# Performance work log

Measured on AMD Instinct MI355X. Metric: run time of the kernel, lower is better.

The kernel has to match this reference:

```python
import jax, jax.numpy as jnp
import numpy as np

DIM = 1024
HEADS = 16
HEAD_DIM = DIM // HEADS


def setup_inputs() -> dict:
    key = jax.random.key(0)
    ks = jax.random.split(key, 9)
    x = jax.random.normal(ks[0], (2, 2048, DIM), dtype=jnp.float32)
    s = 1.0 / np.sqrt(DIM)
    Wq = jax.random.normal(ks[1], (DIM, DIM), dtype=jnp.float32) * s
    bq = jax.random.normal(ks[2], (DIM,), dtype=jnp.float32) * s
    Wk = jax.random.normal(ks[3], (DIM, DIM), dtype=jnp.float32) * s
    bk = jax.random.normal(ks[4], (DIM,), dtype=jnp.float32) * s
    Wv = jax.random.normal(ks[5], (DIM, DIM), dtype=jnp.float32) * s
    bv = jax.random.normal(ks[6], (DIM,), dtype=jnp.float32) * s
    Wo = jax.random.normal(ks[7], (DIM, DIM), dtype=jnp.float32) * s
    bo = jax.random.normal(ks[8], (DIM,), dtype=jnp.float32) * s
    return {"x": x, "Wq": Wq, "bq": bq, "Wk": Wk, "bk": bk,
            "Wv": Wv, "bv": bv, "Wo": Wo, "bo": bo}


def reference(x, Wq, bq, Wk, bk, Wv, bv, Wo, bo):
    B, S, _ = x.shape
    # projections (torch Linear: x @ W.T + b; here W stored as [in, out])
    q = x @ Wq + bq
    k = x @ Wk + bk  # context = x (self-attention)
    v = x @ Wv + bv
    # [B, H, S, Dh]
    q = q.reshape(B, S, HEADS, HEAD_DIM).transpose(0, 2, 1, 3)
    k = k.reshape(B, S, HEADS, HEAD_DIM).transpose(0, 2, 1, 3)
    v = v.reshape(B, S, HEADS, HEAD_DIM).transpose(0, 2, 1, 3)
    scores = jnp.einsum('bhqd,bhkd->bhqk', q, k) / np.sqrt(HEAD_DIM).astype(np.float32)
    weights = jax.nn.softmax(scores, axis=-1)
    emb = jnp.einsum('bhqk,bhkd->bhqd', weights, v)
    emb = emb.transpose(0, 2, 1, 3).reshape(B, S, DIM)
    return emb @ Wo + bo
```

## Files before the change

kernel.cpp:

```cpp
#include <hip/hip_runtime.h>
#include <hip/hip_bf16.h>
#include <stdint.h>

typedef __attribute__((ext_vector_type(8))) short short8;
typedef __attribute__((ext_vector_type(4))) float f32x4;
typedef __attribute__((ext_vector_type(4))) unsigned int uint4v;

#define DIMW 1024
#define HEADS 16
#define HEAD_DIM 64
#define SEQ 2048
#define BATCH 2
#define MTOK 4096
#define QKVN 3072
#define QKN 2048
#define QSCALE 0.1803368801111204f

typedef const __attribute__((address_space(1))) unsigned int* gas_u32p;
typedef __attribute__((address_space(3))) unsigned int* las_u32p;

static __device__ __forceinline__ void gl_lds16(const void* g, void* l) {
    __builtin_amdgcn_global_load_lds((gas_u32p)g, (las_u32p)l, 16, 0, 0);
}

static __device__ __forceinline__ unsigned short f2bf(float f) {
    unsigned int u = __float_as_uint(f);
    u += 0x7fffu + ((u >> 16) & 1u);
    return (unsigned short)(u >> 16);
}

__global__ void cast_x_kernel(const float* __restrict__ x, unsigned short* __restrict__ out) {
    int i = (blockIdx.x * 256 + threadIdx.x) * 8;
    float4 a = *(const float4*)(x + i);
    float4 b = *(const float4*)(x + i + 4);
    unsigned short t[8] = { f2bf(a.x), f2bf(a.y), f2bf(a.z), f2bf(a.w),
                            f2bf(b.x), f2bf(b.y), f2bf(b.z), f2bf(b.w) };
    *(uint4v*)(out + i) = *(const uint4v*)t;
}

__global__ void prep_w_kernel(const float* __restrict__ Wq, const float* __restrict__ Wk,
                              const float* __restrict__ Wv, const float* __restrict__ Wo,
                              unsigned short* __restrict__ Wqkv_t, unsigned short* __restrict__ Wo_t) {
    __shared__ float tile[64][68];
    int z = blockIdx.z;
    const float* W = (z == 0) ? Wq : (z == 1) ? Wk : (z == 2) ? Wv : Wo;
    unsigned short* out = (z < 3) ? (Wqkv_t + (size_t)z * DIMW * DIMW) : Wo_t;
    int n0 = blockIdx.x * 64, k0 = blockIdx.y * 64;
    int tid = threadIdx.x;
    for (int it = 0; it < 4; ++it) {
        int c = it * 256 + tid;
        int r = c >> 4, cg = c & 15;
        float4 v = *(const float4*)(W + (size_t)(k0 + r) * DIMW + n0 + cg * 4);
        tile[r][cg * 4 + 0] = v.x; tile[r][cg * 4 + 1] = v.y;
        tile[r][cg * 4 + 2] = v.z; tile[r][cg * 4 + 3] = v.w;
    }
    __syncthreads();
    for (int it = 0; it < 2; ++it) {
        int c = it * 256 + tid;
        int n = c >> 3, kg = c & 7;
        unsigned short tmp[8];
        #pragma unroll
        for (int j = 0; j < 8; ++j) tmp[j] = f2bf(tile[kg * 8 + j][n]);
        *(uint4v*)(out + (size_t)(n0 + n) * DIMW + k0 + kg * 8) = *(const uint4v*)tmp;
    }
}

template<int MI, bool QKV3, typename TO>
__global__ __launch_bounds__(256, 3) void gemm_bt_kernel(
    const unsigned short* __restrict__ A, const unsigned short* __restrict__ Bt,
    const float* __restrict__ b0, const float* __restrict__ b1, const float* __restrict__ b2,
    TO* __restrict__ C, unsigned short* __restrict__ Vt, int M, int N, int K, int ldc)
{
    __shared__ __align__(16) unsigned short As[MI * 32 * 32];
    __shared__ __align__(16) unsigned short Bs[128 * 32];
    int tid = threadIdx.x;
    int wave = tid >> 6, lane = tid & 63;
    int lrow = lane & 15, quad = lane >> 4;
    int bm = blockIdx.y * (MI * 32), bn = blockIdx.x * 128;
    int wm = (wave >> 1) * (MI * 16), wn = (wave & 1) * 64;
    int sw = (lrow >> 1) & 3;
    f32x4 acc[MI][4];
    #pragma unroll
    for (int i = 0; i < MI; ++i)
        #pragma unroll
        for (int j = 0; j < 4; ++j) acc[i][j] = (f32x4){0.f, 0.f, 0.f, 0.f};
    const unsigned short* Ap = A + (size_t)bm * K;
    const unsigned short* Bp = Bt + (size_t)bn * K;
    for (int k0 = 0; k0 < K; k0 += 32) {
        __syncthreads();
        #pragma unroll
        for (int it = 0; it < MI / 2; ++it) {
            int c = it * 256 + tid;
            int ch = (c & 3) ^ ((c >> 3) & 3);
            gl_lds16(Ap + (size_t)(c >> 2) * K + k0 + ch * 8, &As[c * 8]);
        }
        #pragma unroll
        for (int it = 0; it < 2; ++it) {
            int c = it * 256 + tid;
            int ch = (c & 3) ^ ((c >> 3) & 3);
            gl_lds16(Bp + (size_t)(c >> 2) * K + k0 + ch * 8, &Bs[c * 8]);
        }
        __syncthreads();
        short8 af[MI], bfr[4];
        #pragma unroll
        for (int mi = 0; mi < MI; ++mi)
            af[mi] = *(const short8*)&As[(wm + mi * 16 + lrow) * 32 + (quad ^ sw) * 8];
        #pragma unroll
        for (int ni = 0; ni < 4; ++ni)
            bfr[ni] = *(const short8*)&Bs[(wn + ni * 16 + lrow) * 32 + (quad ^ sw) * 8];
        #pragma unroll
        for (int mi = 0; mi < MI; ++mi)
            #pragma unroll
            for (int ni = 0; ni < 4; ++ni)
                acc[mi][ni] = __builtin_amdgcn_mfma_f32_16x16x32_bf16(af[mi], bfr[ni], acc[mi][ni], 0, 0, 0);
    }
    #pragma unroll
    for (int ni = 0; ni < 4; ++ni) {
        int n = bn + wn + ni * 16 + lrow;
        float bias, scale;
        int sel = 0;
        if (QKV3) {
            sel = n >> 10;
            const float* bp = (sel == 0) ? b0 : (sel == 1) ? b1 : b2;
            bias = bp[n & 1023];
            scale = (sel == 0) ? QSCALE : 1.0f;
        } else { bias = b0[n]; scale = 1.0f; }
        #pragma unroll
        for (int mi = 0; mi < MI; ++mi) {
            int m0 = bm + wm + mi * 16 + quad * 4;
            if (QKV3 && sel == 2) {
                int vcol = n - 2048;
                int bb = m0 >> 11, s0 = m0 & 2047;
                unsigned short t[4];
                #pragma unroll
                for (int i = 0; i < 4; ++i) t[i] = f2bf(acc[mi][ni][i] + bias);
                *(uint2*)(Vt + ((size_t)(bb * 1024 + vcol)) * SEQ + s0) = *(const uint2*)t;
            } else {
                #pragma unroll
                for (int i = 0; i < 4; ++i) {
                    float val = (acc[mi][ni][i] + bias) * scale;
                    if constexpr (sizeof(TO) == 2) C[(size_t)(m0 + i) * ldc + n] = (TO)f2bf(val);
                    else                           C[(size_t)(m0 + i) * ldc + n] = val;
                }
            }
        }
    }
}

__global__ __launch_bounds__(256, 3) void attn_kernel(
    const unsigned short* __restrict__ Qk, const unsigned short* __restrict__ Vt,
    unsigned short* __restrict__ Op, float* __restrict__ L)
{
    __shared__ __align__(16) unsigned short Ks[128 * 64];
    __shared__ __align__(16) unsigned short Vs[64 * 128];
    int tid = threadIdx.x;
    int wave = tid >> 6, lane = tid & 63;
    int lrow = lane & 15, quad = lane >> 4;
    int h = blockIdx.x, qblk = blockIdx.y;
    int b = blockIdx.z >> 1, split = blockIdx.z & 1;
    int q0 = qblk * 128 + wave * 32;
    const unsigned short* Qbase = Qk + (size_t)(b * SEQ) * QKN + h * 64;
    const unsigned short* Kbase = Qk + (size_t)(b * SEQ) * QKN + 1024 + h * 64;
    const unsigned short* Vtb = Vt + (size_t)(b * 1024 + h * 64) * SEQ;

    short8 qf[2][2];
    #pragma unroll
    for (int mi = 0; mi < 2; ++mi)
        #pragma unroll
        for (int kc = 0; kc < 2; ++kc)
            qf[mi][kc] = *(const short8*)(Qbase + (size_t)(q0 + mi * 16 + lrow) * QKN + kc * 32 + quad * 8);

    f32x4 o[2][4];
    float lrun[2] = {0.f, 0.f};
    #pragma unroll
    for (int mi = 0; mi < 2; ++mi)
        #pragma unroll
        for (int ont = 0; ont < 4; ++ont) o[mi][ont] = (f32x4){0.f, 0.f, 0.f, 0.f};

    int kchunk = ((lane & 7) ^ (lane >> 3)) * 8;
    int swk = lrow & 7;

    auto stageK = [&](int kv) {
        #pragma unroll
        for (int it = 0; it < 4; ++it) {
            int r0 = wave * 32 + it * 8;
            gl_lds16(Kbase + (size_t)(kv + r0 + (lane >> 3)) * QKN + kchunk,
                     &Ks[r0 * 64 + lane * 8]);
        }
    };

    int vs_s = lane & 15;
    int vh0 = ((vs_s & 12) << 1) | (vs_s & 3);
    uint2 vreg[8];
    auto loadV = [&](int kv) {
        #pragma unroll
        for (int r = 0; r < 4; ++r) {
            int d = wave * 16 + r * 4 + (lane >> 4);
            const unsigned short* p = Vtb + (size_t)d * SEQ + kv;
            vreg[r * 2]     = *(const uint2*)(p + vh0 * 4);
            vreg[r * 2 + 1] = *(const uint2*)(p + (vh0 + 4) * 4);
        }
    };
    auto writeVs = [&]() {
        #pragma unroll
        for (int r = 0; r < 4; ++r) {
            int d = wave * 16 + r * 4 + (lane >> 4);
            int pos = vs_s ^ (d & 15);
            uint4v w;
            w.x = vreg[r * 2].x;     w.y = vreg[r * 2].y;
            w.z = vreg[r * 2 + 1].x; w.w = vreg[r * 2 + 1].y;
            *(uint4v*)&Vs[d * 128 + pos * 8] = w;
        }
    };

    int kv_lo = split * 1024;
    int kv_end = kv_lo + 1024;

    stageK(kv_lo);
    loadV(kv_lo);
    asm volatile("s_waitcnt vmcnt(0)" ::: "memory");
    __builtin_amdgcn_sched_barrier(0);
    writeVs();

    for (int kv0 = kv_lo; kv0 < kv_end; kv0 += 128) {
        bool has_next = (kv0 + 128) < kv_end;

        __builtin_amdgcn_s_barrier();

        uint4v pav[2][4];
        #pragma unroll
        for (int half = 0; half < 2; ++half) {
            f32x4 s[2][4];
            #pragma unroll
            for (int mi = 0; mi < 2; ++mi)
                #pragma unroll
                for (int nt2 = 0; nt2 < 4; ++nt2) s[mi][nt2] = (f32x4){0.f, 0.f, 0.f, 0.f};
            __builtin_amdgcn_s_setprio(1);
            #pragma unroll
            for (int nt2 = 0; nt2 < 4; ++nt2) {
                int r = (half * 4 + nt2) * 16 + lrow;
                short8 kf0 = *(const short8*)&Ks[r * 64 + (quad ^ swk) * 8];
                short8 kf1 = *(const short8*)&Ks[r * 64 + ((4 + quad) ^ swk) * 8];
                #pragma unroll
                for (int mi = 0; mi < 2; ++mi) {
                    s[mi][nt2] = __builtin_amdgcn_mfma_f32_16x16x32_bf16(kf0, qf[mi][0], s[mi][nt2], 0, 0, 0);
                    s[mi][nt2] = __builtin_amdgcn_mfma_f32_16x16x32_bf16(kf1, qf[mi][1], s[mi][nt2], 0, 0, 0);
                }
            }
            __builtin_amdgcn_s_setprio(0);
            #pragma unroll
            for (int mi = 0; mi < 2; ++mi)
                #pragma unroll
                for (int nt2 = 0; nt2 < 4; ++nt2) {
                    int kt = half * 4 + nt2;
                    f32x4 p;
                    #pragma unroll
                    for (int c2 = 0; c2 < 4; ++c2) {
                        p[c2] = __builtin_amdgcn_exp2f(s[mi][nt2][c2]);
                        lrun[mi] += p[c2];
                    }
                    __hip_bfloat162 a01 = __float22bfloat162_rn(float2{p[0], p[1]});
                    __hip_bfloat162 a23 = __float22bfloat162_rn(float2{p[2], p[3]});
                    if (kt & 1) {
                        pav[mi][kt >> 1].z = *reinterpret_cast<unsigned int*>(&a01);
                        pav[mi][kt >> 1].w = *reinterpret_cast<unsigned int*>(&a23);
                    } else {
                        pav[mi][kt >> 1].x = *reinterpret_cast<unsigned int*>(&a01);
                        pav[mi][kt >> 1].y = *reinterpret_cast<unsigned int*>(&a23);
                    }
                }
        }

        __builtin_amdgcn_s_barrier();

        if (has_next) { stageK(kv0 + 128); loadV(kv0 + 128); }

        #pragma unroll
        for (int kc = 0; kc < 4; ++kc) {
            short8 af0 = *(short8*)&pav[0][kc];
            short8 af1 = *(short8*)&pav[1][kc];
            int pos = ((kc * 4 + quad) ^ lrow) * 8;
            __builtin_amdgcn_s_setprio(1);
            #pragma unroll
            for (int ont = 0; ont < 4; ++ont) {
                int rv = ont * 16 + lrow;
                short8 vf = *(const short8*)&Vs[rv * 128 + pos];
                o[0][ont] = __builtin_amdgcn_mfma_f32_16x16x32_bf16(af0, vf, o[0][ont], 0, 0, 0);
                o[1][ont] = __builtin_amdgcn_mfma_f32_16x16x32_bf16(af1, vf, o[1][ont], 0, 0, 0);
            }
            __builtin_amdgcn_s_setprio(0);
        }

        __builtin_amdgcn_s_barrier();

        if (has_next) {
            asm volatile("s_waitcnt vmcnt(0)" ::: "memory");
            __builtin_amdgcn_sched_barrier(0);
            writeVs();
        }
    }

    #pragma unroll
    for (int mi = 0; mi < 2; ++mi) {
        float l = lrun[mi];
        l += __shfl_xor(l, 16);
        l += __shfl_xor(l, 32);
        #pragma unroll
        for (int ont = 0; ont < 4; ++ont)
            #pragma unroll
            for (int c2 = 0; c2 < 4; ++c2) {
                size_t row = (size_t)((split * 2 + b) * SEQ + q0 + mi * 16 + quad * 4 + c2);
                Op[row * DIMW + h * 64 + ont * 16 + lrow] = f2bf(o[mi][ont][c2]);
            }
        if (quad == 0)
            L[(((size_t)(split * 2 + b) * 16 + h) * SEQ) + q0 + mi * 16 + lrow] = l;
    }
}

__global__ void combine_kernel(const unsigned short* __restrict__ Op,
                               const float* __restrict__ L,
                               unsigned short* __restrict__ Emb)
{
    int e = (blockIdx.x * 256 + threadIdx.x) * 4;
    int row = e >> 10, c = e & 1023, h = c >> 6;
    int b = row >> 11, q = row & 2047;
    float l1 = L[((size_t)(0 + b) * 16 + h) * SEQ + q];
    float l2 = L[((size_t)(2 + b) * 16 + h) * SEQ + q];
    float inv = 1.0f / (l1 + l2);
    uint2 o1 = *(const uint2*)(Op + e);
    uint2 o2 = *(const uint2*)(Op + 4194304 + e);
    unsigned short t[4];
    unsigned int parts1[4] = { o1.x << 16, o1.x & 0xffff0000u, o1.y << 16, o1.y & 0xffff0000u };
    unsigned int parts2[4] = { o2.x << 16, o2.x & 0xffff0000u, o2.y << 16, o2.y & 0xffff0000u };
    #pragma unroll
    for (int j = 0; j < 4; ++j) {
        float f1 = __uint_as_float(parts1[j]);
        float f2 = __uint_as_float(parts2[j]);
        t[j] = f2bf((f1 + f2) * inv);
    }
    *(uint2*)(Emb + e) = *(const uint2*)t;
}

extern "C" void kernel_launch(void* const* d_in, const int* in_sizes, int n_in,
                              void* d_out, int out_size, void* d_ws, size_t ws_size,
                              hipStream_t stream)
{
    const float* x  = (const float*)d_in[0];
    const float* Wq = (const float*)d_in[1];
    const float* bq = (const float*)d_in[2];
    const float* Wk = (const float*)d_in[3];
    const float* bk = (const float*)d_in[4];
    const float* Wv = (const float*)d_in[5];
    const float* bv = (const float*)d_in[6];
    const float* Wo = (const float*)d_in[7];
    const float* bo = (const float*)d_in[8];
    float* out = (float*)d_out;
    char* ws = (char*)d_ws;

    unsigned short* Xbf   = (unsigned short*)(ws);
    unsigned short* Wqkvt = (unsigned short*)(ws + 8388608);
    unsigned short* Wot   = (unsigned short*)(ws + 14680064);
    unsigned short* Qk    = (unsigned short*)(ws + 16777216);
    unsigned short* Vt    = (unsigned short*)(ws + 33554432);
    unsigned short* Emb   = (unsigned short*)(ws + 41943040);
    unsigned short* Op    = (unsigned short*)(ws + 50331648);
    float*          L     = (float*)(ws + 67108864);

    cast_x_kernel<<<2048, 256, 0, stream>>>(x, Xbf);
    prep_w_kernel<<<dim3(16, 16, 4), 256, 0, stream>>>(Wq, Wk, Wv, Wo, Wqkvt, Wot);
    gemm_bt_kernel<4, true, unsigned short><<<dim3(24, 32), 256, 0, stream>>>(
        Xbf, Wqkvt, bq, bk, bv, Qk, Vt, MTOK, QKVN, DIMW, QKN);
    attn_kernel<<<dim3(16, 16, 4), 256, 0, stream>>>(Qk, Vt, Op, L);
    combine_kernel<<<4096, 256, 0, stream>>>(Op, L, Emb);
    gemm_bt_kernel<2, false, float><<<dim3(8, 64), 256, 0, stream>>>(
        Emb, Wot, bo, nullptr, nullptr, out, nullptr, MTOK, DIMW, DIMW, DIMW);
}
```

Measured before the change: 202.2 us.

## Interleave second-half softmax exp with PV MFMAs and issue V load earlier

Restructures the attention inner loop so the second half of the QK^T scores is computed before the barrier, and its exp2/pack work is interleaved with the P·V MFMA steps. The aim is to overlap transcendental VALU work with matrix ops. The next V tile's global load now starts right after the first barrier, so its latency overlaps the QK compute, while the K staging stays after the second barrier. This keeps more score registers live at once, which raises register pressure and could lower occupancy.

```diff
diff --git a/kernel.cpp b/kernel.cpp
--- a/kernel.cpp
+++ b/kernel.cpp
@@ -227,9 +227,11 @@
 
         __builtin_amdgcn_s_barrier();
 
+        if (has_next) loadV(kv0 + 128);
+
         uint4v pav[2][4];
-        #pragma unroll
-        for (int half = 0; half < 2; ++half) {
+
+        {
             f32x4 s[2][4];
             #pragma unroll
             for (int mi = 0; mi < 2; ++mi)
@@ -238,7 +240,7 @@
             __builtin_amdgcn_s_setprio(1);
             #pragma unroll
             for (int nt2 = 0; nt2 < 4; ++nt2) {
-                int r = (half * 4 + nt2) * 16 + lrow;
+                int r = nt2 * 16 + lrow;
                 short8 kf0 = *(const short8*)&Ks[r * 64 + (quad ^ swk) * 8];
                 short8 kf1 = *(const short8*)&Ks[r * 64 + ((4 + quad) ^ swk) * 8];
                 #pragma unroll
@@ -252,31 +254,66 @@
             for (int mi = 0; mi < 2; ++mi)
                 #pragma unroll
                 for (int nt2 = 0; nt2 < 4; ++nt2) {
-                    int kt = half * 4 + nt2;
                     f32x4 p;
                     #pragma unroll
-                    for (int c2 = 0; c2 < 4; ++c2) {
-                        p[c2] = __builtin_amdgcn_exp2f(s[mi][nt2][c2]);
-                        lrun[mi] += p[c2];
-                    }
+                    for (int c2 = 0; c2 < 4; ++c2) p[c2] = __builtin_amdgcn_exp2f(s[mi][nt2][c2]);
+                    lrun[mi] += (p[0] + p[1]) + (p[2] + p[3]);
                     __hip_bfloat162 a01 = __float22bfloat162_rn(float2{p[0], p[1]});
                     __hip_bfloat162 a23 = __float22bfloat162_rn(float2{p[2], p[3]});
-                    if (kt & 1) {
-                        pav[mi][kt >> 1].z = *reinterpret_cast<unsigned int*>(&a01);
-                        pav[mi][kt >> 1].w = *reinterpret_cast<unsigned int*>(&a23);
+                    if (nt2 & 1) {
+                        pav[mi][nt2 >> 1].z = *reinterpret_cast<unsigned int*>(&a01);
+                        pav[mi][nt2 >> 1].w = *reinterpret_cast<unsigned int*>(&a23);
                     } else {
-                        pav[mi][kt >> 1].x = *reinterpret_cast<unsigned int*>(&a01);
-                        pav[mi][kt >> 1].y = *reinterpret_cast<unsigned int*>(&a23);
+                        pav[mi][nt2 >> 1].x = *reinterpret_cast<unsigned int*>(&a01);
+                        pav[mi][nt2 >> 1].y = *reinterpret_cast<unsigned int*>(&a23);
                     }
                 }
         }
 
+        f32x4 s1[2][4];
+        {
+            #pragma unroll
+            for (int mi = 0; mi < 2; ++mi)
+                #pragma unroll
+                for (int nt2 = 0; nt2 < 4; ++nt2) s1[mi][nt2] = (f32x4){0.f, 0.f, 0.f, 0.f};
+            __builtin_amdgcn_s_setprio(1);
+            #pragma unroll
+            for (int nt2 = 0; nt2 < 4; ++nt2) {
+                int r = (4 + nt2) * 16 + lrow;
+                short8 kf0 = *(const short8*)&Ks[r * 64 + (quad ^ swk) * 8];
+                short8 kf1 = *(const short8*)&Ks[r * 64 + ((4 + quad) ^ swk) * 8];
+                #pragma unroll
+                for (int mi = 0; mi < 2; ++mi) {
+                    s1[mi][nt2] = __builtin_amdgcn_mfma_f32_16x16x32_bf16(kf0, qf[mi][0], s1[mi][nt2], 0, 0, 0);
+                    s1[mi][nt2] = __builtin_amdgcn_mfma_f32_16x16x32_bf16(kf1, qf[mi][1], s1[mi][nt2], 0, 0, 0);
+                }
+            }
+            __builtin_amdgcn_s_setprio(0);
+        }
+
         __builtin_amdgcn_s_barrier();
 
-        if (has_next) { stageK(kv0 + 128); loadV(kv0 + 128); }
-
-        #pragma unroll
-        for (int kc = 0; kc < 4; ++kc) {
+        if (has_next) stageK(kv0 + 128);
+
+        auto expPack1 = [&](int nt2) {
+            #pragma unroll
+            for (int mi = 0; mi < 2; ++mi) {
+                f32x4 p;
+                #pragma unroll
+                for (int c2 = 0; c2 < 4; ++c2) p[c2] = __builtin_amdgcn_exp2f(s1[mi][nt2][c2]);
+                lrun[mi] += (p[0] + p[1]) + (p[2] + p[3]);
+                __hip_bfloat162 a01 = __float22bfloat162_rn(float2{p[0], p[1]});
+                __hip_bfloat162 a23 = __float22bfloat162_rn(float2{p[2], p[3]});
+                if (nt2 & 1) {
+                    pav[mi][2 + (nt2 >> 1)].z = *reinterpret_cast<unsigned int*>(&a01);
+                    pav[mi][2 + (nt2 >> 1)].w = *reinterpret_cast<unsigned int*>(&a23);
+                } else {
+                    pav[mi][2 + (nt2 >> 1)].x = *reinterpret_cast<unsigned int*>(&a01);
+                    pav[mi][2 + (nt2 >> 1)].y = *reinterpret_cast<unsigned int*>(&a23);
+                }
+            }
+        };
+        auto pvStep = [&](int kc) {
             short8 af0 = *(short8*)&pav[0][kc];
             short8 af1 = *(short8*)&pav[1][kc];
             int pos = ((kc * 4 + quad) ^ lrow) * 8;
@@ -289,7 +326,16 @@
                 o[1][ont] = __builtin_amdgcn_mfma_f32_16x16x32_bf16(af1, vf, o[1][ont], 0, 0, 0);
             }
             __builtin_amdgcn_s_setprio(0);
-        }
+        };
+
+        expPack1(0);
+        expPack1(1);
+        pvStep(0);
+        expPack1(2);
+        expPack1(3);
+        pvStep(1);
+        pvStep(2);
+        pvStep(3);
 
         __builtin_amdgcn_s_barrier();
 
```

Result: no change. 199.3 us (-1.4%).
